# Kernel optimization log

Hardware: AMD Instinct MI355X
Metric: run time of the kernel (lower is better)

Reference implementation:

```python
import jax, jax.numpy as jnp
import numpy as np

# Static graph layout: 64 equal-size graphs so per-graph k is static (jit-friendly).
B = 64          # number of graphs
N_PER = 4096    # nodes per graph (batch vector is sorted, equal blocks)
N = B * N_PER   # 262144 total nodes
C = 128         # in_channels
E = 4194304     # number of edges (avg degree 16)
RATIO = 0.8
K = int(np.ceil(RATIO * N_PER))  # 3277 nodes kept per graph


def setup_inputs() -> dict:
    key = jax.random.key(0)
    k1, k2, k3 = jax.random.split(key, 3)
    x = jax.random.normal(k1, (N, C), dtype=jnp.float32)
    # learned projection (torch init is zeros; use small randn so scores are non-degenerate)
    coefficient = jax.random.normal(k2, (C, 1), dtype=jnp.float32) * 0.1
    edge_index = jax.random.randint(k3, (2, E), 0, N, dtype=jnp.int32)
    # sorted, equal-size graph assignment (matches torch_geometric batch convention)
    batch = jnp.repeat(jnp.arange(B, dtype=jnp.int32), N_PER)
    return {"x": x, "coefficient": coefficient, "edge_index": edge_index, "batch": batch}


def reference(x, coefficient, edge_index, batch):
    # score = x @ coefficient, squeezed -> [N]
    score = (x @ coefficient)[:, 0]

    # topk(): per-graph descending sort + take top ceil(ratio*n) nodes.
    # Equal-size sorted graphs -> dense view is a plain reshape; lax.top_k gives
    # descending-sorted indices per graph, matching torch's dense sort+mask path.
    dense = score.reshape(B, N_PER)              # [B, N_PER]
    _, idx = jax.lax.top_k(dense, K)             # [B, K] local indices, score-descending
    offsets = (jnp.arange(B, dtype=idx.dtype) * N_PER)[:, None]
    perm = (idx + offsets).reshape(-1)           # [B*K] global node indices

    # gather nodes, gate by sigmoid(score)
    gate = jax.nn.sigmoid(score[perm])           # [B*K]
    x_pooled = x[perm] * gate[:, None]           # [B*K, C]
    batch_pooled = batch[perm]

    # filter_adj: relabel kept nodes 0..B*K-1, drop edges with a removed endpoint.
    node_map = jnp.full((N,), -1, dtype=jnp.int32)
    node_map = node_map.at[perm].set(jnp.arange(perm.shape[0], dtype=jnp.int32))
    row = node_map[edge_index[0]]
    col = node_map[edge_index[1]]
    valid = (row >= 0) & (col >= 0)              # [E]
    # static-shape equivalent of torch's dynamic edge filtering: stable-sort valid
    # edges to the front (preserving original order), pad invalid slots with -1.
    order = jnp.argsort(jnp.logical_not(valid), stable=True)
    new_edge_index = jnp.stack([row, col])[:, order]
    new_edge_index = jnp.where(valid[order][None, :], new_edge_index, -1)

    return (x_pooled, new_edge_index, batch_pooled, perm)
```

## Files before the change

### kernel.cpp

```cpp
#include <hip/hip_runtime.h>
#include <hip/hip_bf16.h>

#define BG    64
#define NPER  4096
#define NTOT  (BG * NPER)
#define CC    128
#define EE    4194304
#define KK    3277
#define BK    (BG * KK)
#define NBLK  512
#define EPB   8192

#define OFF_X     0
#define OFF_EDGE  (BK * CC)
#define OFF_BATCH (OFF_EDGE + 2 * EE)
#define OFF_PERM  (OFF_BATCH + BK)

#define CH0_BYTES  ((size_t)OFF_EDGE * 4)
#define A_OFF_B    (CH0_BYTES - (size_t)NTOT * 4)
#define BM_OFF_B   (A_OFF_B - 32768)
#define LP_OFF_B   (BM_OFF_B - 16384)
#define BO_OFF_B   (LP_OFF_B - 8192)
#define BC_OFF_B   (LP_OFF_B - 16384)
#define CTRL_OFF_B (LP_OFF_B - 16640)
#define PAIRS_OFF_B (CTRL_OFF_B - (size_t)EE * 4)

typedef unsigned long long u64;

static __device__ __forceinline__ unsigned short bf16_bits(float f) {
    __hip_bfloat16 h = __float2bfloat16(f);
    return *reinterpret_cast<unsigned short*>(&h);
}
static __device__ __forceinline__ unsigned obf(float v) {
    return ((unsigned)bf16_bits(v)) << 16;
}
static __device__ __forceinline__ unsigned ald(const unsigned* p) {
    return __hip_atomic_load(p, __ATOMIC_ACQUIRE, __HIP_MEMORY_SCOPE_AGENT);
}
static __device__ __forceinline__ void ast(unsigned* p, unsigned v) {
    __hip_atomic_store(p, v, __ATOMIC_RELEASE, __HIP_MEMORY_SCOPE_AGENT);
}

__global__ void score_kernel(const float* __restrict__ x,
                             const float* __restrict__ coef,
                             float* __restrict__ arr_f,
                             unsigned* __restrict__ ctrl) {
    if (blockIdx.x == 0 && threadIdx.x < 2) ast(&ctrl[threadIdx.x], 0u);

    int lane = threadIdx.x & 63;
    int half = lane >> 5;
    int cg   = lane & 31;
    int waveId = (blockIdx.x * blockDim.x + threadIdx.x) >> 6;
    int nWaves = (gridDim.x * blockDim.x) >> 6;

    float4 c = ((const float4*)coef)[cg];

    for (int pair = waveId; pair < NTOT / 2; pair += nWaves) {
        int row = 2 * pair + half;
        float4 v = ((const float4*)(x + (size_t)row * CC))[cg];
        double s = (double)v.x * c.x + (double)v.y * c.y
                 + (double)v.z * c.z + (double)v.w * c.w;
        #pragma unroll
        for (int off = 16; off > 0; off >>= 1)
            s += __shfl_xor(s, off, 64);
        if (cg == 0) arr_f[row] = (float)s;
    }
}

__global__ __launch_bounds__(512) void topk_kernel(const float* __restrict__ arr_f,
                                                   unsigned* __restrict__ st_li,
                                                   unsigned* __restrict__ st_gate,
                                                   unsigned* __restrict__ bm_g,
                                                   unsigned short* __restrict__ lp_g) {
    __shared__ unsigned hist[2048];
    __shared__ unsigned sScan[512];
    __shared__ unsigned sSel[2];
    __shared__ unsigned sTie[128];
    __shared__ unsigned lbm[128];
    __shared__ unsigned lpc[128];

    int b = blockIdx.x, t = threadIdx.x;
    const float* s = arr_f + (b << 12);

    float4 v0 = *(const float4*)(s + (t << 3));
    float4 v1 = *(const float4*)(s + (t << 3) + 4);
    float vv[8] = {v0.x, v0.y, v0.z, v0.w, v1.x, v1.y, v1.z, v1.w};
    unsigned key[8];
    #pragma unroll
    for (int m = 0; m < 8; ++m) {
        unsigned u = __float_as_uint(vv[m]);
        u = u ^ ((u >> 31) ? 0xFFFFFFFFu : 0x80000000u);
        key[m] = ~u;
    }

    unsigned need = KK;

    for (int i = t; i < 2048; i += 512) hist[i] = 0;
    __syncthreads();
    #pragma unroll
    for (int m = 0; m < 8; ++m) atomicAdd(&hist[key[m] >> 21], 1u);
    __syncthreads();
    {
        unsigned c0 = hist[t*4], c1 = hist[t*4+1], c2 = hist[t*4+2], c3 = hist[t*4+3];
        unsigned s4 = c0 + c1 + c2 + c3;
        sScan[t] = s4; __syncthreads();
        #pragma unroll
        for (int off = 1; off < 512; off <<= 1) {
            unsigned add = (t >= off) ? sScan[t-off] : 0u; __syncthreads();
            sScan[t] += add; __syncthreads();
        }
        unsigned excl = sScan[t] - s4;
        if (excl < need && need <= sScan[t]) {
            unsigned cum = excl, bin = t*4u;
            if      (cum + c0 >= need)           { sSel[0]=bin;   sSel[1]=cum; }
            else if (cum + c0 + c1 >= need)      { sSel[0]=bin+1; sSel[1]=cum+c0; }
            else if (cum + c0 + c1 + c2 >= need) { sSel[0]=bin+2; sSel[1]=cum+c0+c1; }
            else                                 { sSel[0]=bin+3; sSel[1]=cum+c0+c1+c2; }
        }
        __syncthreads();
    }
    unsigned B1 = sSel[0]; need -= sSel[1];
    __syncthreads();

    for (int i = t; i < 2048; i += 512) hist[i] = 0;
    __syncthreads();
    #pragma unroll
    for (int m = 0; m < 8; ++m)
        if ((key[m] >> 21) == B1) atomicAdd(&hist[(key[m] >> 10) & 2047u], 1u);
    __syncthreads();
    {
        unsigned c0 = hist[t*4], c1 = hist[t*4+1], c2 = hist[t*4+2], c3 = hist[t*4+3];
        unsigned s4 = c0 + c1 + c2 + c3;
        sScan[t] = s4; __syncthreads();
        #pragma unroll
        for (int off = 1; off < 512; off <<= 1) {
            unsigned add = (t >= off) ? sScan[t-off] : 0u; __syncthreads();
            sScan[t] += add; __syncthreads();
        }
        unsigned excl = sScan[t] - s4;
        if (excl < need && need <= sScan[t]) {
            unsigned cum = excl, bin = t*4u;
            if      (cum + c0 >= need)           { sSel[0]=bin;   sSel[1]=cum; }
            else if (cum + c0 + c1 >= need)      { sSel[0]=bin+1; sSel[1]=cum+c0; }
            else if (cum + c0 + c1 + c2 >= need) { sSel[0]=bin+2; sSel[1]=cum+c0+c1; }
            else                                 { sSel[0]=bin+3; sSel[1]=cum+c0+c1+c2; }
        }
        __syncthreads();
    }
    unsigned B2 = sSel[0]; need -= sSel[1];
    unsigned P2 = (B1 << 11) | B2;
    __syncthreads();

    for (int i = t; i < 2048; i += 512) hist[i] = 0;
    __syncthreads();
    #pragma unroll
    for (int m = 0; m < 8; ++m)
        if ((key[m] >> 10) == P2) atomicAdd(&hist[key[m] & 1023u], 1u);
    __syncthreads();
    {
        unsigned c0 = hist[t*2], c1 = hist[t*2+1];
        unsigned s2 = c0 + c1;
        sScan[t] = s2; __syncthreads();
        #pragma unroll
        for (int off = 1; off < 512; off <<= 1) {
            unsigned add = (t >= off) ? sScan[t-off] : 0u; __syncthreads();
            sScan[t] += add; __syncthreads();
        }
        unsigned excl = sScan[t] - s2;
        if (excl < need && need <= sScan[t]) {
            if (excl + c0 >= need) { sSel[0] = t*2u;   sSel[1] = excl; }
            else                   { sSel[0] = t*2u+1; sSel[1] = excl + c0; }
        }
        __syncthreads();
    }
    unsigned KSTAR = (P2 << 10) | sSel[0];
    unsigned needT = need - sSel[1];
    __syncthreads();

    if (t < 128) sTie[t] = 0;
    __syncthreads();
    #pragma unroll
    for (int m = 0; m < 8; ++m) {
        if (key[m] == KSTAR) {
            unsigned idx = (unsigned)((t << 3) | m);
            atomicOr(&sTie[idx >> 5], 1u << (idx & 31));
        }
    }
    __syncthreads();
    if (t == 0) {
        unsigned rem = needT, it = 0;
        for (int w = 0; w < 128; ++w) {
            unsigned word = sTie[w], pc = __popc(word);
            if (rem <= pc) {
                for (unsigned bit = 0; ; ++bit)
                    if ((word >> bit) & 1u) { if (--rem == 0) { it = w*32u + bit; break; } }
                break;
            }
            rem -= pc;
        }
        sSel[0] = it;
    }
    __syncthreads();
    unsigned idxT = sSel[0];

    if (t < 128) lbm[t] = 0u;
    __syncthreads();
    unsigned kmask = 0;
    #pragma unroll
    for (int m = 0; m < 8; ++m) {
        unsigned idx = (unsigned)((t << 3) | m);
        bool kept = (key[m] < KSTAR) || (key[m] == KSTAR && idx <= idxT);
        if (kept) { kmask |= 1u << m; atomicOr(&lbm[idx >> 5], 1u << (idx & 31)); }
    }
    __syncthreads();
    if (t < 128) lpc[t] = __popc(lbm[t]);
    __syncthreads();
    #pragma unroll
    for (int off = 1; off < 128; off <<= 1) {
        unsigned add = (t < 128 && t >= off) ? lpc[t - off] : 0u;
        __syncthreads();
        if (t < 128) lpc[t] += add;
        __syncthreads();
    }
    if (t < 128) {
        unsigned w = lbm[t];
        bm_g[(b << 7) + t] = w;
        lp_g[(b << 7) + t] = (unsigned short)(lpc[t] - __popc(w));
    }
    #pragma unroll
    for (int m = 0; m < 8; ++m) {
        if ((kmask >> m) & 1u) {
            unsigned idx = (unsigned)((t << 3) | m);
            unsigned w = lbm[idx >> 5];
            unsigned p = (lpc[idx >> 5] - __popc(w))
                       + (unsigned)__popc(w & ((1u << (idx & 31)) - 1u));
            int j = b * KK + (int)p;
            float gate = 1.0f / (1.0f + expf(-vv[m]));
            st_li[j]   = idx;
            st_gate[j] = __float_as_uint(gate);
        }
    }
}

__global__ __launch_bounds__(512, 4) void edge_pass1(
        const int* __restrict__ edge,
        const unsigned* __restrict__ bm_g,
        const unsigned short* __restrict__ lp_g,
        unsigned* __restrict__ pairs,
        unsigned* __restrict__ counts,
        unsigned* __restrict__ prefix,
        unsigned* __restrict__ ctrl) {
    __shared__ unsigned sBm[8192];
    __shared__ unsigned short sLp[8192];
    __shared__ unsigned sWaveSum[8];
    __shared__ unsigned sScan[512];
    __shared__ int sTicket;

    int b = blockIdx.x;
    int base = b << 13;
    int tid = threadIdx.x;
    int lane = tid & 63, wid = tid >> 6;
    u64 lmask = (1ull << lane) - 1ull;

    for (int i = tid; i < 8192; i += 512) sBm[i] = bm_g[i];
    for (int i = tid; i < 4096; i += 512)
        ((unsigned*)sLp)[i] = ((const unsigned*)lp_g)[i];
    __syncthreads();

    int chunk = base + (wid << 10);

    int ev0[16], ev1[16];
    #pragma unroll
    for (int k = 0; k < 16; ++k) ev0[k] = edge[chunk + (k << 6) + lane];
    #pragma unroll
    for (int k = 0; k < 16; ++k) ev1[k] = edge[EE + chunk + (k << 6) + lane];

    u64 bal[16];
    unsigned pk[16];
    unsigned cnt = 0;
    #pragma unroll
    for (int k = 0; k < 16; ++k) {
        int u0i = ev0[k], u1i = ev1[k];
        unsigned w0 = sBm[u0i >> 5], w1 = sBm[u1i >> 5];
        bool valid = ((w0 >> (u0i & 31)) & (w1 >> (u1i & 31)) & 1u) != 0u;
        bal[k] = __ballot(valid);
        unsigned pkk = 0;
        if (valid) {
            unsigned j0 = (unsigned)(u0i >> 12) * KK + sLp[u0i >> 5]
                        + (unsigned)__popc(w0 & ((1u << (u0i & 31)) - 1u));
            unsigned j1 = (unsigned)(u1i >> 12) * KK + sLp[u1i >> 5]
                        + (unsigned)__popc(w1 & ((1u << (u1i & 31)) - 1u));
            pkk = obf((float)j0) | (unsigned)bf16_bits((float)j1);
        }
        pk[k] = pkk;
        cnt += (unsigned)__popcll(bal[k]);
    }

    if (lane == 0) sWaveSum[wid] = cnt;
    __syncthreads();

    unsigned waveBase = 0, run = 0;
    #pragma unroll
    for (int w = 0; w < 8; ++w) {
        unsigned s = sWaveSum[w];
        if (w < wid) waveBase += s;
        run += s;
    }

    unsigned* pb = pairs + base;
    unsigned wrun = 0;
    #pragma unroll
    for (int k = 0; k < 16; ++k) {
        if ((bal[k] >> lane) & 1ull) {
            unsigned pos = waveBase + wrun + (unsigned)__popcll(bal[k] & lmask);
            pb[pos] = pk[k];
        }
        wrun += (unsigned)__popcll(bal[k]);
    }

    if (tid == 0) {
        ast(&counts[b], run);
        sTicket = (int)__hip_atomic_fetch_add(&ctrl[0], 1u, __ATOMIC_ACQ_REL,
                                              __HIP_MEMORY_SCOPE_AGENT);
    }
    __syncthreads();

    if (sTicket == NBLK - 1) {
        unsigned v = ald(&counts[tid]);
        sScan[tid] = v;
        __syncthreads();
        #pragma unroll
        for (int off = 1; off < 512; off <<= 1) {
            unsigned add = (tid >= off) ? sScan[tid - off] : 0u;
            __syncthreads();
            sScan[tid] += add;
            __syncthreads();
        }
        prefix[tid] = sScan[tid] - v;
        if (tid == 511) prefix[NBLK] = sScan[511];
    }
}

__global__ __launch_bounds__(256) void edge_pass2(
        const unsigned* __restrict__ pairs,
        const unsigned* __restrict__ prefix,
        unsigned* __restrict__ out32) {
    int b = blockIdx.x;
    unsigned base = (unsigned)(b << 13);
    unsigned tid = threadIdx.x;
    unsigned blockOff = prefix[b];
    unsigned cnt = prefix[b + 1] - blockOff;
    unsigned nvalid = prefix[NBLK];
    unsigned* oe = out32 + OFF_EDGE;
    const unsigned* pb = pairs + base;

    for (unsigned i = tid; i < cnt; i += 256u) {
        unsigned w = pb[i];
        oe[blockOff + i]      = w & 0xFFFF0000u;
        oe[EE + blockOff + i] = w << 16;
    }
    unsigned tailBase = nvalid + base - blockOff;
    unsigned tcnt = (unsigned)EPB - cnt;
    unsigned NEG1 = obf(-1.0f);
    for (unsigned i = tid; i < tcnt; i += 256u) {
        oe[tailBase + i]      = NEG1;
        oe[EE + tailBase + i] = NEG1;
    }
}

__global__ void gather_kernel(const float* __restrict__ x,
                              const unsigned* __restrict__ st_li,
                              const unsigned* __restrict__ st_gate,
                              unsigned* __restrict__ out32) {
    int tid = blockIdx.x * blockDim.x + threadIdx.x;
    int rowsPerGrid = (gridDim.x * blockDim.x) >> 5;
    int rid = tid >> 5;
    int cg  = tid & 31;

    for (int row = rid; row < BK; row += rowsPerGrid) {
        int b  = row / KK;
        int li = (int)st_li[row];
        int node = (b << 12) + li;
        float g = __uint_as_float(st_gate[row]);
        float4 v = ((const float4*)(x + (size_t)node * CC))[cg];
        uint4 o;
        o.x = obf(v.x * g);
        o.y = obf(v.y * g);
        o.z = obf(v.z * g);
        o.w = obf(v.w * g);
        ((uint4*)(out32 + OFF_X))[(size_t)row * 32 + cg] = o;
        if (cg == 0) {
            out32[OFF_BATCH + row] = obf((float)b);
            out32[OFF_PERM + row]  = obf((float)node);
        }
    }
}

extern "C" void kernel_launch(void* const* d_in, const int* in_sizes, int n_in,
                              void* d_out, int out_size, void* d_ws, size_t ws_size,
                              hipStream_t stream) {
    const float* x    = nullptr;
    const float* coef = nullptr;
    const int*   edge = nullptr;
    for (int i = 0; i < n_in; ++i) {
        switch (in_sizes[i]) {
            case NTOT * CC: x    = (const float*)d_in[i]; break;
            case CC:        coef = (const float*)d_in[i]; break;
            case 2 * EE:    edge = (const int*)d_in[i];   break;
            default: break;
        }
    }
    if (!x || !coef || !edge) return;

    char* ob = (char*)d_out;
    unsigned* out32 = (unsigned*)d_out;
    float*          A      = (float*)(ob + A_OFF_B);
    unsigned*       bm_g   = (unsigned*)(ob + BM_OFF_B);
    unsigned short* lp_g   = (unsigned short*)(ob + LP_OFF_B);
    unsigned*       counts = (unsigned*)(ob + BC_OFF_B);
    unsigned*       prefix = (unsigned*)(ob + BO_OFF_B);
    unsigned*       ctrl   = (unsigned*)(ob + CTRL_OFF_B);
    unsigned*       pairs  = (unsigned*)(ob + PAIRS_OFF_B);
    unsigned* st_li   = out32 + OFF_BATCH;
    unsigned* st_gate = out32 + OFF_PERM;

    score_kernel<<<2048, 256, 0, stream>>>(x, coef, A, ctrl);
    topk_kernel<<<BG, 512, 0, stream>>>(A, st_li, st_gate, bm_g, lp_g);
    edge_pass1<<<NBLK, 512, 0, stream>>>(edge, bm_g, lp_g, pairs, counts,
                                         prefix, ctrl);
    edge_pass2<<<NBLK, 256, 0, stream>>>(pairs, prefix, out32);
    gather_kernel<<<4096, 256, 0, stream>>>(x, st_li, st_gate, out32);
}
```

Before: 141.1 us.

## Compact edges per wave segment to drop intra-block barrier in edge pass

Edge compaction now treats each 1024-edge wave chunk as its own segment, with per-wave counts and a 4096-entry prefix scan, in place of per-block counts. This removes the block-wide barrier and the held ballot and packed arrays in pass1, which lowers register pressure, and the launch-bounds occupancy hint is dropped. Pass2 becomes one wave per segment at 512 threads per block. The costs are a larger scan in the last block and shorter contiguous write runs per segment.

```diff
diff --git a/kernel.cpp b/kernel.cpp
--- a/kernel.cpp
+++ b/kernel.cpp
@@ -9,7 +9,7 @@
 #define KK    3277
 #define BK    (BG * KK)
 #define NBLK  512
-#define EPB   8192
+#define NSEG  4096
 
 #define OFF_X     0
 #define OFF_EDGE  (BK * CC)
@@ -20,9 +20,9 @@
 #define A_OFF_B    (CH0_BYTES - (size_t)NTOT * 4)
 #define BM_OFF_B   (A_OFF_B - 32768)
 #define LP_OFF_B   (BM_OFF_B - 16384)
-#define BO_OFF_B   (LP_OFF_B - 8192)
-#define BC_OFF_B   (LP_OFF_B - 16384)
-#define CTRL_OFF_B (LP_OFF_B - 16640)
+#define BO_OFF_B   (LP_OFF_B - 20480)
+#define BC_OFF_B   (BO_OFF_B - 16384)
+#define CTRL_OFF_B (BC_OFF_B - 256)
 #define PAIRS_OFF_B (CTRL_OFF_B - (size_t)EE * 4)
 
 typedef unsigned long long u64;
@@ -242,7 +242,7 @@
     }
 }
 
-__global__ __launch_bounds__(512, 4) void edge_pass1(
+__global__ __launch_bounds__(512) void edge_pass1(
         const int* __restrict__ edge,
         const unsigned* __restrict__ bm_g,
         const unsigned short* __restrict__ lp_g,
@@ -252,12 +252,10 @@
         unsigned* __restrict__ ctrl) {
     __shared__ unsigned sBm[8192];
     __shared__ unsigned short sLp[8192];
-    __shared__ unsigned sWaveSum[8];
     __shared__ unsigned sScan[512];
     __shared__ int sTicket;
 
     int b = blockIdx.x;
-    int base = b << 13;
     int tid = threadIdx.x;
     int lane = tid & 63, wid = tid >> 6;
     u64 lmask = (1ull << lane) - 1ull;
@@ -267,7 +265,8 @@
         ((unsigned*)sLp)[i] = ((const unsigned*)lp_g)[i];
     __syncthreads();
 
-    int chunk = base + (wid << 10);
+    int seg = (b << 3) + wid;
+    int chunk = seg << 10;
 
     int ev0[16], ev1[16];
     #pragma unroll
@@ -275,59 +274,37 @@
     #pragma unroll
     for (int k = 0; k < 16; ++k) ev1[k] = edge[EE + chunk + (k << 6) + lane];
 
-    u64 bal[16];
-    unsigned pk[16];
-    unsigned cnt = 0;
+    unsigned* ps = pairs + ((size_t)seg << 10);
+    unsigned wrun = 0;
     #pragma unroll
     for (int k = 0; k < 16; ++k) {
         int u0i = ev0[k], u1i = ev1[k];
         unsigned w0 = sBm[u0i >> 5], w1 = sBm[u1i >> 5];
         bool valid = ((w0 >> (u0i & 31)) & (w1 >> (u1i & 31)) & 1u) != 0u;
-        bal[k] = __ballot(valid);
-        unsigned pkk = 0;
+        u64 bal = __ballot(valid);
         if (valid) {
             unsigned j0 = (unsigned)(u0i >> 12) * KK + sLp[u0i >> 5]
                         + (unsigned)__popc(w0 & ((1u << (u0i & 31)) - 1u));
             unsigned j1 = (unsigned)(u1i >> 12) * KK + sLp[u1i >> 5]
                         + (unsigned)__popc(w1 & ((1u << (u1i & 31)) - 1u));
-            pkk = obf((float)j0) | (unsigned)bf16_bits((float)j1);
-        }
-        pk[k] = pkk;
-        cnt += (unsigned)__popcll(bal[k]);
-    }
-
-    if (lane == 0) sWaveSum[wid] = cnt;
-    __syncthreads();
-
-    unsigned waveBase = 0, run = 0;
-    #pragma unroll
-    for (int w = 0; w < 8; ++w) {
-        unsigned s = sWaveSum[w];
-        if (w < wid) waveBase += s;
-        run += s;
-    }
-
-    unsigned* pb = pairs + base;
-    unsigned wrun = 0;
-    #pragma unroll
-    for (int k = 0; k < 16; ++k) {
-        if ((bal[k] >> lane) & 1ull) {
-            unsigned pos = waveBase + wrun + (unsigned)__popcll(bal[k] & lmask);
-            pb[pos] = pk[k];
-        }
-        wrun += (unsigned)__popcll(bal[k]);
-    }
-
-    if (tid == 0) {
-        ast(&counts[b], run);
+            ps[wrun + (unsigned)__popcll(bal & lmask)] =
+                obf((float)j0) | (unsigned)bf16_bits((float)j1);
+        }
+        wrun += (unsigned)__popcll(bal);
+    }
+    if (lane == 0) ast(&counts[seg], wrun);
+    __syncthreads();
+
+    if (tid == 0)
         sTicket = (int)__hip_atomic_fetch_add(&ctrl[0], 1u, __ATOMIC_ACQ_REL,
                                               __HIP_MEMORY_SCOPE_AGENT);
-    }
     __syncthreads();
 
     if (sTicket == NBLK - 1) {
-        unsigned v = ald(&counts[tid]);
-        sScan[tid] = v;
+        unsigned v[8]; unsigned s8 = 0;
+        #pragma unroll
+        for (int i = 0; i < 8; ++i) { v[i] = ald(&counts[tid*8+i]); s8 += v[i]; }
+        sScan[tid] = s8;
         __syncthreads();
         #pragma unroll
         for (int off = 1; off < 512; off <<= 1) {
@@ -336,33 +313,37 @@
             sScan[tid] += add;
             __syncthreads();
         }
-        prefix[tid] = sScan[tid] - v;
-        if (tid == 511) prefix[NBLK] = sScan[511];
-    }
-}
-
-__global__ __launch_bounds__(256) void edge_pass2(
+        unsigned run = sScan[tid] - s8;
+        #pragma unroll
+        for (int i = 0; i < 8; ++i) { prefix[tid*8+i] = run; run += v[i]; }
+        if (tid == 511) prefix[NSEG] = run;
+    }
+}
+
+__global__ __launch_bounds__(512) void edge_pass2(
         const unsigned* __restrict__ pairs,
         const unsigned* __restrict__ prefix,
         unsigned* __restrict__ out32) {
     int b = blockIdx.x;
-    unsigned base = (unsigned)(b << 13);
-    unsigned tid = threadIdx.x;
-    unsigned blockOff = prefix[b];
-    unsigned cnt = prefix[b + 1] - blockOff;
-    unsigned nvalid = prefix[NBLK];
+    int tid = threadIdx.x;
+    int lane = tid & 63, wid = tid >> 6;
+    int seg = (b << 3) + wid;
+    unsigned segBase = (unsigned)(seg << 10);
+    unsigned off = prefix[seg];
+    unsigned cnt = prefix[seg + 1] - off;
+    unsigned nvalid = prefix[NSEG];
     unsigned* oe = out32 + OFF_EDGE;
-    const unsigned* pb = pairs + base;
-
-    for (unsigned i = tid; i < cnt; i += 256u) {
-        unsigned w = pb[i];
-        oe[blockOff + i]      = w & 0xFFFF0000u;
-        oe[EE + blockOff + i] = w << 16;
-    }
-    unsigned tailBase = nvalid + base - blockOff;
-    unsigned tcnt = (unsigned)EPB - cnt;
+    const unsigned* ps = pairs + segBase;
+
+    for (unsigned i = (unsigned)lane; i < cnt; i += 64u) {
+        unsigned w = ps[i];
+        oe[off + i]      = w & 0xFFFF0000u;
+        oe[EE + off + i] = w << 16;
+    }
+    unsigned tailBase = nvalid + segBase - off;
+    unsigned tcnt = 1024u - cnt;
     unsigned NEG1 = obf(-1.0f);
-    for (unsigned i = tid; i < tcnt; i += 256u) {
+    for (unsigned i = (unsigned)lane; i < tcnt; i += 64u) {
         oe[tailBase + i]      = NEG1;
         oe[EE + tailBase + i] = NEG1;
     }
@@ -417,8 +398,8 @@
     float*          A      = (float*)(ob + A_OFF_B);
     unsigned*       bm_g   = (unsigned*)(ob + BM_OFF_B);
     unsigned short* lp_g   = (unsigned short*)(ob + LP_OFF_B);
+    unsigned*       prefix = (unsigned*)(ob + BO_OFF_B);
     unsigned*       counts = (unsigned*)(ob + BC_OFF_B);
-    unsigned*       prefix = (unsigned*)(ob + BO_OFF_B);
     unsigned*       ctrl   = (unsigned*)(ob + CTRL_OFF_B);
     unsigned*       pairs  = (unsigned*)(ob + PAIRS_OFF_B);
     unsigned* st_li   = out32 + OFF_BATCH;
@@ -428,6 +409,6 @@
     topk_kernel<<<BG, 512, 0, stream>>>(A, st_li, st_gate, bm_g, lp_g);
     edge_pass1<<<NBLK, 512, 0, stream>>>(edge, bm_g, lp_g, pairs, counts,
                                          prefix, ctrl);
-    edge_pass2<<<NBLK, 256, 0, stream>>>(pairs, prefix, out32);
+    edge_pass2<<<NBLK, 512, 0, stream>>>(pairs, prefix, out32);
     gather_kernel<<<4096, 256, 0, stream>>>(x, st_li, st_gate, out32);
 }
```

After: 183.4 us. 1.3x slower.
